# Optimization experiments

Hardware: AMD Instinct MI355X
Metric: run time of the kernel (lower is better)

Reference implementation:

```python
import jax, jax.numpy as jnp
import numpy as np

C = 128  # n_atom_basis


def setup_inputs() -> dict:
    key = jax.random.key(0)
    k_h, k_A, k_Ww, k_Wb, k_aw, k_ab = jax.random.split(key, 6)
    B, N = 8, 2048
    h = jax.random.normal(k_h, (B, N, C), dtype=jnp.float32)
    A = jax.random.uniform(k_A, (B, N, N), dtype=jnp.float32)
    # nn.Linear(C, C)
    lim_W = 1.0 / np.sqrt(C)
    W_w = jax.random.uniform(k_Ww, (C, C), minval=-lim_W, maxval=lim_W, dtype=jnp.float32)
    W_b = jax.random.uniform(k_Wb, (C,), minval=-lim_W, maxval=lim_W, dtype=jnp.float32)
    # nn.Linear(2C, 1)
    lim_a = 1.0 / np.sqrt(2 * C)
    a_w = jax.random.uniform(k_aw, (2 * C,), minval=-lim_a, maxval=lim_a, dtype=jnp.float32)
    a_b = jax.random.uniform(k_ab, (), minval=-lim_a, maxval=lim_a, dtype=jnp.float32)
    return {"h": h, "A": A, "W_w": W_w, "W_b": W_b, "a_w": a_w, "a_b": a_b}


def reference(h, A, W_w, W_b, a_w, a_b):
    # Wh computed once ([B,N,C]) instead of the original's redundant [B,N,N,C] broadcast.
    Wh = jnp.einsum('bnc,dc->bnd', h, W_w) + W_b
    # a([hi, hj]) = a_w[:C]@Wh_i + a_w[C:]@Wh_j + a_b  -> rank-1 decomposition of the concat-linear
    si = Wh @ a_w[:C]          # [B,N]
    sj = Wh @ a_w[C:]          # [B,N]
    s = si[:, :, None] + sj[:, None, :] + a_b  # [B,N,N] raw scores
    e = jnp.exp(s) * A                          # masked exp (no max-subtraction: matches original math)
    alpha = e / jnp.sum(e, axis=2, keepdims=True)
    # weighted sum over neighbors j of the ORIGINAL h (as in the source, not Wh)
    h_prime = jnp.einsum('bij,bjc->bic', alpha, h)
    return h_prime
```

## Files before the change

kernel.cpp:

```cpp
#include <hip/hip_runtime.h>
#include <math.h>
#include <stdint.h>

#define Bn 8
#define Nn 2048
#define Cn 128
#define CP 144
#define NKB (Nn / 32)

typedef _Float16 f16x8 __attribute__((ext_vector_type(8)));
typedef _Float16 f16x4 __attribute__((ext_vector_type(4)));
typedef _Float16 f16x2 __attribute__((ext_vector_type(2)));
typedef __fp16   fp16x2 __attribute__((ext_vector_type(2)));
typedef float    f32x4 __attribute__((ext_vector_type(4)));

__global__ __launch_bounds__(256) void rows_kernel(const float* __restrict__ h,
                                                   const float* __restrict__ Ww,
                                                   const float* __restrict__ Wb,
                                                   const float* __restrict__ aw,
                                                   _Float16* __restrict__ hWt) {
    __shared__ float tile[16][132];
    __shared__ float vlo[128];
    __shared__ float vhi[128];
    __shared__ float wsh[16];
    __shared__ float b2sh;

    int bid = blockIdx.x;
    int b   = bid & 7;
    int n0  = (bid >> 3) << 4;
    int tid = threadIdx.x;

    {
        int c = tid & 127, half = tid >> 7;
        float acc = 0.f;
#pragma unroll
        for (int dd = 0; dd < 64; ++dd) {
            int d = half * 64 + dd;
            acc += Ww[d * Cn + c] * aw[Cn + d];
        }
        if (half) vhi[c] = acc; else vlo[c] = acc;
    }
    if (tid < 64) {
        float b2p = Wb[tid] * aw[Cn + tid] + Wb[tid + 64] * aw[Cn + tid + 64];
        b2p += __shfl_xor(b2p, 32, 64);
        b2p += __shfl_xor(b2p, 16, 64);
        b2p += __shfl_xor(b2p, 8, 64);
        b2p += __shfl_xor(b2p, 4, 64);
        b2p += __shfl_xor(b2p, 2, 64);
        b2p += __shfl_xor(b2p, 1, 64);
        if (tid == 0) b2sh = b2p;
    }
    {
#pragma unroll
        for (int i = 0; i < 2; ++i) {
            int idx = tid + 256 * i;
            int r = idx >> 5, f4 = idx & 31;
            *(float4*)&tile[r][f4 * 4] =
                ((const float4*)(h + (size_t)(b * Nn + n0 + r) * Cn))[f4];
        }
    }
    __syncthreads();

    {
        int r = tid >> 4, g = tid & 15;
        float acc = 0.f;
#pragma unroll
        for (int ii = 0; ii < 8; ++ii) {
            int i = g * 8 + ii;
            acc += tile[r][i] * (vlo[i] + vhi[i]);
        }
        acc += __shfl_xor(acc, 1, 64);
        acc += __shfl_xor(acc, 2, 64);
        acc += __shfl_xor(acc, 4, 64);
        acc += __shfl_xor(acc, 8, 64);
        if (g == 0) wsh[r] = expf(acc + b2sh);
    }
    __syncthreads();

    {
        int kb = n0 >> 5, khalf = (n0 >> 4) & 1;
        _Float16* hWb = hWt + ((size_t)(b * NKB + kb) * CP) * 32 + khalf * 16;
#pragma unroll
        for (int i = 0; i < 5; ++i) {
            int idx = tid + 256 * i;
            if (idx < 1152) {
                int cp = idx >> 3, p = idx & 7;
                int r0 = p * 2;
                f16x2 v2;
                if (cp < 128) {
                    v2[0] = (_Float16)(wsh[r0] * tile[r0][cp]);
                    v2[1] = (_Float16)(wsh[r0 + 1] * tile[r0 + 1][cp]);
                } else if (cp == 128) {
                    v2[0] = (_Float16)wsh[r0];
                    v2[1] = (_Float16)wsh[r0 + 1];
                } else {
                    v2[0] = (_Float16)0.f;
                    v2[1] = (_Float16)0.f;
                }
                *(f16x2*)(hWb + (size_t)cp * 32 + p * 2) = v2;
            }
        }
    }
}

__global__ __launch_bounds__(512, 4) void attn_kernel(const float* __restrict__ A,
                                                      const _Float16* __restrict__ hWt,
                                                      float* __restrict__ out) {
    __shared__ _Float16 Af[2][2][32][40];
    __shared__ float den[32];

    int bid = blockIdx.x;
    int b   = bid & 7;
    int i0  = (bid >> 3) << 5;
    int tid = threadIdx.x;
    int wv  = tid >> 6, l = tid & 63;
    int m   = l & 15, q = l >> 4;

    const float*    Ab  = A   + (size_t)(b * Nn + i0) * Nn;
    const _Float16* hWb = hWt + (size_t)b * NKB * CP * 32;

    int sr = tid >> 4, sf4 = tid & 15;
    const float* sg = Ab + (size_t)sr * Nn + sf4 * 4;
    int sch = sf4 >> 3, skl = (sf4 & 7) * 4;

    f32x4 accc[2];
    f32x4 acc8;
    accc[0] = (f32x4){0.f, 0.f, 0.f, 0.f};
    accc[1] = (f32x4){0.f, 0.f, 0.f, 0.f};
    acc8    = (f32x4){0.f, 0.f, 0.f, 0.f};

    auto loadA = [&](int t) { return *(const float4*)(sg + t * 64); };
    auto storeA = [&](int t, float4 v) {
        union { fp16x2 h2[2]; f16x4 v4; } u;
        u.h2[0] = __builtin_amdgcn_cvt_pkrtz(v.x, v.y);
        u.h2[1] = __builtin_amdgcn_cvt_pkrtz(v.z, v.w);
        *(f16x4*)&Af[t & 1][sch][sr][skl] = u.v4;
    };
    auto loadB = [&](int t, f16x8* bf) {
#pragma unroll
        for (int ck = 0; ck < 2; ++ck)
            bf[ck] = *(const f16x8*)(hWb + ((size_t)(2 * t + ck) * CP + wv * 16 + m) * 32 + q * 8);
        if (wv < 2) {
#pragma unroll
            for (int ck = 0; ck < 2; ++ck)
                bf[2 + ck] = *(const f16x8*)(hWb + ((size_t)(2 * t + ck) * CP + 128 + m) * 32 + q * 8);
        }
    };
    auto compute = [&](int buf, const f16x8* bf) {
#pragma unroll
        for (int ck = 0; ck < 2; ++ck) {
            f16x8 af0 = *(const f16x8*)&Af[buf][ck][m][q * 8];
            f16x8 af1 = *(const f16x8*)&Af[buf][ck][16 + m][q * 8];
            accc[0] = __builtin_amdgcn_mfma_f32_16x16x32_f16(af0, bf[ck], accc[0], 0, 0, 0);
            accc[1] = __builtin_amdgcn_mfma_f32_16x16x32_f16(af1, bf[ck], accc[1], 0, 0, 0);
            if (wv < 2)
                acc8 = __builtin_amdgcn_mfma_f32_16x16x32_f16(wv ? af1 : af0, bf[2 + ck],
                                                              acc8, 0, 0, 0);
        }
    };

    float4 a0 = loadA(0);
    float4 a1 = loadA(1);
    f16x8 bfA[4], bfB[4];
    loadB(0, bfA);
    storeA(0, a0);
    __syncthreads();

    for (int t2 = 0; t2 < 16; ++t2) {
        int te = 2 * t2, to = te + 1;
        loadB(to, bfB);
        if (t2 < 15) a0 = loadA(te + 2);
        compute(0, bfA);
        storeA(to, a1);
        __syncthreads();
        if (t2 < 15) {
            loadB(to + 1, bfA);
            a1 = loadA(to + 2);
        }
        compute(1, bfB);
        if (t2 < 15) storeA(to + 1, a0);
        __syncthreads();
    }

    if (wv < 2 && m == 0) {
#pragma unroll
        for (int r = 0; r < 4; ++r) den[wv * 16 + q * 4 + r] = acc8[r];
    }
    __syncthreads();

#pragma unroll
    for (int mt = 0; mt < 2; ++mt) {
#pragma unroll
        for (int r = 0; r < 4; ++r) {
            int row = mt * 16 + q * 4 + r;
            float invd = 1.f / den[row];
            out[(size_t)(b * Nn + i0 + row) * Cn + wv * 16 + m] = accc[mt][r] * invd;
        }
    }
}

extern "C" void kernel_launch(void* const* d_in, const int* in_sizes, int n_in,
                              void* d_out, int out_size, void* d_ws, size_t ws_size,
                              hipStream_t stream) {
    const float* h  = (const float*)d_in[0];
    const float* A  = (const float*)d_in[1];
    const float* Ww = (const float*)d_in[2];
    const float* Wb = (const float*)d_in[3];
    const float* aw = (const float*)d_in[4];
    float* out = (float*)d_out;

    _Float16* hWt = (_Float16*)d_ws;

    rows_kernel<<<Bn * (Nn / 16), 256, 0, stream>>>(h, Ww, Wb, aw, hWt);
    attn_kernel<<<Bn * (Nn / 32), 512, 0, stream>>>(A, hWt, out);
}
```

Before: 226.0 us.

## Double attention K-step per stage and hoist weight-vector precompute into prep kernel

The attention kernel now processes 128 columns of A per pipeline stage instead of 64, so each thread loads two rows of A per stage, the LDS buffer doubles, and the main loop runs half as many iterations with half as many barriers. The projected-weight vector and bias term were recomputed by every rows_kernel block; they are now computed once by a single-block prep kernel and read from workspace. The trade is more registers for the B fragments and more LDS per block, which may reduce occupancy, plus one extra kernel launch.

```diff
diff --git a/kernel.cpp b/kernel.cpp
--- a/kernel.cpp
+++ b/kernel.cpp
@@ -14,42 +14,42 @@
 typedef __fp16   fp16x2 __attribute__((ext_vector_type(2)));
 typedef float    f32x4 __attribute__((ext_vector_type(4)));
 
-__global__ __launch_bounds__(256) void rows_kernel(const float* __restrict__ h,
-                                                   const float* __restrict__ Ww,
+__global__ __launch_bounds__(256) void prep_kernel(const float* __restrict__ Ww,
                                                    const float* __restrict__ Wb,
                                                    const float* __restrict__ aw,
+                                                   float* __restrict__ vout) {
+    int tid = threadIdx.x;
+    if (tid < 128) {
+        float acc = 0.f;
+#pragma unroll 16
+        for (int d = 0; d < Cn; ++d) acc += Ww[d * Cn + tid] * aw[Cn + d];
+        vout[tid] = acc;
+    } else if (tid < 192) {
+        int i = tid - 128;
+        float p = Wb[i] * aw[Cn + i] + Wb[i + 64] * aw[Cn + i + 64];
+        p += __shfl_xor(p, 32, 64);
+        p += __shfl_xor(p, 16, 64);
+        p += __shfl_xor(p, 8, 64);
+        p += __shfl_xor(p, 4, 64);
+        p += __shfl_xor(p, 2, 64);
+        p += __shfl_xor(p, 1, 64);
+        if (i == 0) vout[128] = p;
+    }
+}
+
+__global__ __launch_bounds__(256) void rows_kernel(const float* __restrict__ h,
+                                                   const float* __restrict__ vout,
                                                    _Float16* __restrict__ hWt) {
     __shared__ float tile[16][132];
-    __shared__ float vlo[128];
-    __shared__ float vhi[128];
+    __shared__ float vsh[129];
     __shared__ float wsh[16];
-    __shared__ float b2sh;
 
     int bid = blockIdx.x;
     int b   = bid & 7;
     int n0  = (bid >> 3) << 4;
     int tid = threadIdx.x;
 
-    {
-        int c = tid & 127, half = tid >> 7;
-        float acc = 0.f;
-#pragma unroll
-        for (int dd = 0; dd < 64; ++dd) {
-            int d = half * 64 + dd;
-            acc += Ww[d * Cn + c] * aw[Cn + d];
-        }
-        if (half) vhi[c] = acc; else vlo[c] = acc;
-    }
-    if (tid < 64) {
-        float b2p = Wb[tid] * aw[Cn + tid] + Wb[tid + 64] * aw[Cn + tid + 64];
-        b2p += __shfl_xor(b2p, 32, 64);
-        b2p += __shfl_xor(b2p, 16, 64);
-        b2p += __shfl_xor(b2p, 8, 64);
-        b2p += __shfl_xor(b2p, 4, 64);
-        b2p += __shfl_xor(b2p, 2, 64);
-        b2p += __shfl_xor(b2p, 1, 64);
-        if (tid == 0) b2sh = b2p;
-    }
+    if (tid < 129) vsh[tid] = vout[tid];
     {
 #pragma unroll
         for (int i = 0; i < 2; ++i) {
@@ -67,13 +67,13 @@
 #pragma unroll
         for (int ii = 0; ii < 8; ++ii) {
             int i = g * 8 + ii;
-            acc += tile[r][i] * (vlo[i] + vhi[i]);
+            acc += tile[r][i] * vsh[i];
         }
         acc += __shfl_xor(acc, 1, 64);
         acc += __shfl_xor(acc, 2, 64);
         acc += __shfl_xor(acc, 4, 64);
         acc += __shfl_xor(acc, 8, 64);
-        if (g == 0) wsh[r] = expf(acc + b2sh);
+        if (g == 0) wsh[r] = expf(acc + vsh[128]);
     }
     __syncthreads();
 
@@ -106,7 +106,7 @@
 __global__ __launch_bounds__(512, 4) void attn_kernel(const float* __restrict__ A,
                                                       const _Float16* __restrict__ hWt,
                                                       float* __restrict__ out) {
-    __shared__ _Float16 Af[2][2][32][40];
+    __shared__ _Float16 Af[2][4][32][40];
     __shared__ float den[32];
 
     int bid = blockIdx.x;
@@ -119,8 +119,9 @@
     const float*    Ab  = A   + (size_t)(b * Nn + i0) * Nn;
     const _Float16* hWb = hWt + (size_t)b * NKB * CP * 32;
 
-    int sr = tid >> 4, sf4 = tid & 15;
-    const float* sg = Ab + (size_t)sr * Nn + sf4 * 4;
+    int sr0 = tid >> 5, sf4 = tid & 31;
+    const float* sgA = Ab + (size_t)sr0 * Nn + sf4 * 4;
+    const float* sgB = Ab + (size_t)(sr0 + 16) * Nn + sf4 * 4;
     int sch = sf4 >> 3, skl = (sf4 & 7) * 4;
 
     f32x4 accc[2];
@@ -129,56 +130,66 @@
     accc[1] = (f32x4){0.f, 0.f, 0.f, 0.f};
     acc8    = (f32x4){0.f, 0.f, 0.f, 0.f};
 
-    auto loadA = [&](int t) { return *(const float4*)(sg + t * 64); };
-    auto storeA = [&](int t, float4 v) {
+    auto cvtst = [&](int t, int row, float4 v) {
         union { fp16x2 h2[2]; f16x4 v4; } u;
         u.h2[0] = __builtin_amdgcn_cvt_pkrtz(v.x, v.y);
         u.h2[1] = __builtin_amdgcn_cvt_pkrtz(v.z, v.w);
-        *(f16x4*)&Af[t & 1][sch][sr][skl] = u.v4;
+        *(f16x4*)&Af[t & 1][sch][row][skl] = u.v4;
     };
     auto loadB = [&](int t, f16x8* bf) {
 #pragma unroll
-        for (int ck = 0; ck < 2; ++ck)
-            bf[ck] = *(const f16x8*)(hWb + ((size_t)(2 * t + ck) * CP + wv * 16 + m) * 32 + q * 8);
+        for (int ck = 0; ck < 4; ++ck)
+            bf[ck] = *(const f16x8*)(hWb + ((size_t)(4 * t + ck) * CP + wv * 16 + m) * 32 + q * 8);
         if (wv < 2) {
 #pragma unroll
-            for (int ck = 0; ck < 2; ++ck)
-                bf[2 + ck] = *(const f16x8*)(hWb + ((size_t)(2 * t + ck) * CP + 128 + m) * 32 + q * 8);
+            for (int ck = 0; ck < 4; ++ck)
+                bf[4 + ck] = *(const f16x8*)(hWb + ((size_t)(4 * t + ck) * CP + 128 + m) * 32 + q * 8);
         }
     };
     auto compute = [&](int buf, const f16x8* bf) {
 #pragma unroll
-        for (int ck = 0; ck < 2; ++ck) {
+        for (int ck = 0; ck < 4; ++ck) {
             f16x8 af0 = *(const f16x8*)&Af[buf][ck][m][q * 8];
             f16x8 af1 = *(const f16x8*)&Af[buf][ck][16 + m][q * 8];
             accc[0] = __builtin_amdgcn_mfma_f32_16x16x32_f16(af0, bf[ck], accc[0], 0, 0, 0);
             accc[1] = __builtin_amdgcn_mfma_f32_16x16x32_f16(af1, bf[ck], accc[1], 0, 0, 0);
             if (wv < 2)
-                acc8 = __builtin_amdgcn_mfma_f32_16x16x32_f16(wv ? af1 : af0, bf[2 + ck],
+                acc8 = __builtin_amdgcn_mfma_f32_16x16x32_f16(wv ? af1 : af0, bf[4 + ck],
                                                               acc8, 0, 0, 0);
         }
     };
 
-    float4 a0 = loadA(0);
-    float4 a1 = loadA(1);
-    f16x8 bfA[4], bfB[4];
+    float4 a0x = *(const float4*)(sgA);
+    float4 a0y = *(const float4*)(sgB);
+    float4 a1x = *(const float4*)(sgA + 128);
+    float4 a1y = *(const float4*)(sgB + 128);
+    f16x8 bfA[8], bfB[8];
     loadB(0, bfA);
-    storeA(0, a0);
-    __syncthreads();
-
-    for (int t2 = 0; t2 < 16; ++t2) {
+    cvtst(0, sr0, a0x);
+    cvtst(0, sr0 + 16, a0y);
+    __syncthreads();
+
+    for (int t2 = 0; t2 < 8; ++t2) {
         int te = 2 * t2, to = te + 1;
         loadB(to, bfB);
-        if (t2 < 15) a0 = loadA(te + 2);
+        if (t2 < 7) {
+            a0x = *(const float4*)(sgA + (te + 2) * 128);
+            a0y = *(const float4*)(sgB + (te + 2) * 128);
+        }
         compute(0, bfA);
-        storeA(to, a1);
+        cvtst(to, sr0, a1x);
+        cvtst(to, sr0 + 16, a1y);
         __syncthreads();
-        if (t2 < 15) {
+        if (t2 < 7) {
             loadB(to + 1, bfA);
-            a1 = loadA(to + 2);
+            a1x = *(const float4*)(sgA + (to + 2) * 128);
+            a1y = *(const float4*)(sgB + (to + 2) * 128);
         }
         compute(1, bfB);
-        if (t2 < 15) storeA(to + 1, a0);
+        if (t2 < 7) {
+            cvtst(to + 1, sr0, a0x);
+            cvtst(to + 1, sr0 + 16, a0y);
+        }
         __syncthreads();
     }
 
@@ -209,8 +220,11 @@
     const float* aw = (const float*)d_in[4];
     float* out = (float*)d_out;
 
-    _Float16* hWt = (_Float16*)d_ws;
-
-    rows_kernel<<<Bn * (Nn / 16), 256, 0, stream>>>(h, Ww, Wb, aw, hWt);
+    char* ws = (char*)d_ws;
+    _Float16* hWt  = (_Float16*)ws;
+    float*    vout = (float*)(ws + (size_t)Bn * NKB * CP * 32 * 2);
+
+    prep_kernel<<<1, 256, 0, stream>>>(Ww, Wb, aw, vout);
+    rows_kernel<<<Bn * (Nn / 16), 256, 0, stream>>>(h, vout, hWt);
     attn_kernel<<<Bn * (Nn / 32), 512, 0, stream>>>(A, hWt, out);
 }
```

Measured after the change: 234.8 us. 3.9% more time.
